# Optimization experiments

Measured on AMD Instinct MI355X. Metric: run time of the kernel, lower is better.

## Reference

```python
import jax, jax.numpy as jnp
import numpy as np
import math

B, S, D, O_DIM = 8, 2048, 1024, 1024

def setup_inputs() -> dict:
    key = jax.random.key(0)
    ks = jax.random.split(key, 4)
    scale = 1.0 / math.sqrt(D)
    return {
        "x": jax.random.normal(ks[0], (B, S, D), dtype=jnp.float32),
        "Wq": jax.random.normal(ks[1], (D, O_DIM), dtype=jnp.float32) * scale,
        "bq": jnp.zeros((O_DIM,), dtype=jnp.float32),
        "Wk": jax.random.normal(ks[2], (D, O_DIM), dtype=jnp.float32) * scale,
        "bk": jnp.zeros((O_DIM,), dtype=jnp.float32),
        "Wv": jax.random.normal(ks[3], (D, O_DIM), dtype=jnp.float32) * scale,
        "bv": jnp.zeros((O_DIM,), dtype=jnp.float32),
    }

def reference(x, Wq, bq, Wk, bk, Wv, bv):
    o_dim = Wq.shape[1]
    q = x @ Wq + bq  # [B,S,O]
    k = x @ Wk + bk
    v = x @ Wv + bv
    scores = jnp.einsum('bid,bjd->bij', q, k) / jnp.sqrt(jnp.float32(o_dim))
    n = scores.shape[1]
    # causal additive mask: upper triangle (j > i) gets -1e20 added
    causal = jnp.tril(jnp.ones((n, n), dtype=scores.dtype))
    scores = scores + (1.0 - causal) * (-1e20)
    probs = jax.nn.softmax(scores, axis=-1)
    return jnp.einsum('bij,bjd->bid', probs, v)
```

## Files before the change

### kernel.cpp

```cpp
#include <hip/hip_runtime.h>

#define BM 128
#define BN 128
#define BK 32

typedef unsigned short u16;
typedef unsigned int u32;
typedef __attribute__((ext_vector_type(8))) short short8;
typedef __attribute__((ext_vector_type(4))) float floatx4;

__device__ __forceinline__ u16 f2bf(float f) {
  u32 u = __float_as_uint(f);
  return (u16)((u + 0x7FFFu + ((u >> 16) & 1u)) >> 16);
}

__device__ __forceinline__ float bf2f(u16 b) {
  return __uint_as_float(((u32)b) << 16);
}

__device__ __forceinline__ void gload16(const void* g, void* l) {
  __builtin_amdgcn_global_load_lds((const __attribute__((address_space(1))) void*)g,
                                   (__attribute__((address_space(3))) void*)l, 16, 0, 0);
}

template<int BIAS_MODE, int SWZ>
__global__ __launch_bounds__(512, 2)
void gemm256(const u16* __restrict__ A, int lda,
             const u16* __restrict__ B, int ldb,
             u16* __restrict__ C, int ldc,
             const float* __restrict__ bias, int K)
{
  int bx = blockIdx.x, by = blockIdx.y;
  if (SWZ == 1) {
    const int c = gridDim.x >> 3;
    bx = (bx & 7) * c + (bx >> 3);
  } else if (SWZ == 2) {
    const u32 gx = gridDim.x;
    const u32 flat = (u32)by * gx + (u32)bx;
    const u32 j = flat & 7u, w = flat >> 3;
    const u32 rpx = gridDim.y >> 3;
    by = (int)(j * rpx + w / gx);
    bx = (int)(w % gx);
  }
  const int rb = by * 256, cb = bx * 256;

  __shared__ __align__(16) char lds[131072];

  const int t = threadIdx.x;
  const int lane = t & 63, wid = t >> 6;
  const int wr = wid >> 2, wc = wid & 3;

  floatx4 acc[8][4];
#pragma unroll
  for (int i = 0; i < 8; ++i)
#pragma unroll
    for (int j = 0; j < 4; ++j) acc[i][j] = (floatx4)(0.0f);

  const int sr = t >> 2;
  const int sl = (t & 3) ^ ((sr >> 1) & 3);
  const u16* Ag0 = A + (long)(rb + sr) * lda + sl * 8;
  const u16* Ag1 = A + (long)(rb + sr + 128) * lda + sl * 8;
  const u16* Bg0 = B + (long)(cb + sr) * ldb + sl * 8;
  const u16* Bg1 = B + (long)(cb + sr + 128) * ldb + sl * 8;

#define STAGE_A(T) { const long ko_ = (long)(T) * 32;                          \
    char* d_ = lds + (((T) & 3) << 15) + (wid << 10);                          \
    gload16(Ag0 + ko_, d_); gload16(Ag1 + ko_, d_ + 8192); }
#define STAGE_B(T) { const long ko_ = (long)(T) * 32;                          \
    char* d_ = lds + (((T) & 3) << 15) + 16384 + (wid << 10);                  \
    gload16(Bg0 + ko_, d_); gload16(Bg1 + ko_, d_ + 8192); }

  const int g = lane >> 4;
  int aoff[8], boff[4];
  const int arow = wr * 128 + (lane & 15);
  const int brow = wc * 64 + (lane & 15);
#pragma unroll
  for (int i = 0; i < 8; ++i) {
    const int ra = arow + i * 16;
    aoff[i] = ra * 64 + ((g ^ ((ra >> 1) & 3)) * 16);
  }
#pragma unroll
  for (int j = 0; j < 4; ++j) {
    const int rbq = brow + j * 16;
    boff[j] = rbq * 64 + ((g ^ ((rbq >> 1) & 3)) * 16);
  }

  const int NT = K / 32;

  STAGE_A(0); STAGE_B(0);
  STAGE_A(1); STAGE_B(1);
  STAGE_A(2); STAGE_B(2);
  asm volatile("s_waitcnt vmcnt(8)" ::: "memory");
  __builtin_amdgcn_s_barrier();
  asm volatile("" ::: "memory");

  for (int T = 0; T < NT; ++T) {
    const char* bufA = lds + ((T & 3) << 15);
    const char* bufB = bufA + 16384;

    if (T + 3 < NT) STAGE_A(T + 3);
    short8 a0[4], bfr[4];
#pragma unroll
    for (int i = 0; i < 4; ++i) a0[i] = *(const short8*)(bufA + aoff[i]);
#pragma unroll
    for (int j = 0; j < 4; ++j) bfr[j] = *(const short8*)(bufB + boff[j]);
    __builtin_amdgcn_s_setprio(1);
#pragma unroll
    for (int mi = 0; mi < 4; ++mi)
#pragma unroll
      for (int nj = 0; nj < 4; ++nj)
        acc[mi][nj] = __builtin_amdgcn_mfma_f32_16x16x32_bf16(a0[mi], bfr[nj], acc[mi][nj], 0, 0, 0);
    __builtin_amdgcn_s_setprio(0);

    if (T + 3 < NT) STAGE_B(T + 3);
    short8 a1[4];
#pragma unroll
    for (int i = 0; i < 4; ++i) a1[i] = *(const short8*)(bufA + aoff[4 + i]);
    __builtin_amdgcn_s_setprio(1);
#pragma unroll
    for (int mi = 0; mi < 4; ++mi)
#pragma unroll
      for (int nj = 0; nj < 4; ++nj)
        acc[4 + mi][nj] = __builtin_amdgcn_mfma_f32_16x16x32_bf16(a1[mi], bfr[nj], acc[4 + mi][nj], 0, 0, 0);
    __builtin_amdgcn_s_setprio(0);

    asm volatile("" ::: "memory");
    if (T < NT - 3) {
      asm volatile("s_waitcnt vmcnt(8)" ::: "memory");
      __builtin_amdgcn_s_barrier();
    } else if (T == NT - 3) {
      asm volatile("s_waitcnt vmcnt(4)" ::: "memory");
      __builtin_amdgcn_s_barrier();
    } else if (T == NT - 2) {
      asm volatile("s_waitcnt vmcnt(0)" ::: "memory");
      __builtin_amdgcn_s_barrier();
    }
    asm volatile("" ::: "memory");
  }
#undef STAGE_A
#undef STAGE_B

#pragma unroll
  for (int mi = 0; mi < 8; ++mi) {
    const int r0 = rb + wr * 128 + mi * 16 + (lane >> 4) * 4;
#pragma unroll
    for (int nj = 0; nj < 4; ++nj) {
      const int c = cb + wc * 64 + nj * 16 + (lane & 15);
      float bc = 0.0f;
      if (BIAS_MODE == 1) bc = bias[c];
#pragma unroll
      for (int e = 0; e < 4; ++e) {
        const int r = r0 + e;
        float val = acc[mi][nj][e] + bc;
        if (BIAS_MODE == 2) val += bias[r];
        C[(long)r * ldc + c] = f2bf(val);
      }
    }
  }
}

template<int BIAS_MODE, bool OUT_BF16, bool CAUSAL, bool KLIMIT, int SWZ>
__global__ __launch_bounds__(256)
void gemm_nt(const u16* __restrict__ A, int lda, long strideA,
             const u16* __restrict__ B, int ldb, long strideB,
             void* __restrict__ Cv, int ldc, long strideC,
             const float* __restrict__ bias, float scale,
             int M, int N, int K)
{
  int bx = blockIdx.x;
  int by = blockIdx.y;
  if (SWZ == 1) {
    const int c = gridDim.x >> 3;
    bx = (bx & 7) * c + (bx >> 3);
  } else if (SWZ == 2) {
    const u32 gx = gridDim.x;
    const u32 flat = (u32)by * gx + (u32)bx;
    const u32 j = flat & 7u;
    const u32 w = flat >> 3;
    const u32 rpx = gridDim.y >> 3;
    by = (int)(j * rpx + w / gx);
    bx = (int)(w % gx);
  } else if (SWZ == 3) {
    by = gridDim.y - 1 - by;
  }
  const int rb = by * BM;
  const int cb = bx * BN;
  if (CAUSAL && cb > rb + (BM - 1)) return;

  A += (long)blockIdx.z * strideA;
  B += (long)blockIdx.z * strideB;
  const long coff = (long)blockIdx.z * strideC;

  __shared__ u16 As[BM * BK];
  __shared__ u16 Bs[BN * BK];

  const int t = threadIdx.x;
  const int lane = t & 63;
  const int wid = t >> 6;
  const int wr = wid >> 1, wc = wid & 1;

  floatx4 acc[4][4];
#pragma unroll
  for (int i = 0; i < 4; ++i)
#pragma unroll
    for (int j = 0; j < 4; ++j) acc[i][j] = (floatx4)(0.0f);

  const int srow = t >> 2;
  const int schunk = (t & 3) ^ ((srow >> 1) & 3);
  const u16* Ag0 = A + (long)(rb + srow) * lda + schunk * 8;
  const u16* Ag1 = A + (long)(rb + srow + 64) * lda + schunk * 8;
  const u16* Bg0 = B + (long)(cb + srow) * ldb + schunk * 8;
  const u16* Bg1 = B + (long)(cb + srow + 64) * ldb + schunk * 8;
  char* AsW = (char*)As + wid * 1024;
  char* BsW = (char*)Bs + wid * 1024;

  const int arow = wr * 64 + (lane & 15);
  const int brow = wc * 64 + (lane & 15);
  const int rchunk = lane >> 4;
  int aoff[4], boff[4];
#pragma unroll
  for (int i = 0; i < 4; ++i) {
    const int ra = arow + i * 16;
    aoff[i] = ra * 64 + ((rchunk ^ ((ra >> 1) & 3)) * 16);
    const int rbq = brow + i * 16;
    boff[i] = rbq * 64 + ((rchunk ^ ((rbq >> 1) & 3)) * 16);
  }

  int kend = K;
  if (KLIMIT) kend = (rb + BM < K) ? (rb + BM) : K;
  const int ktiles = kend / BK;

  for (int kt = 0; kt < ktiles; ++kt) {
    const long ko = (long)kt * BK;
    gload16(Ag0 + ko, AsW);
    gload16(Ag1 + ko, AsW + 4096);
    gload16(Bg0 + ko, BsW);
    gload16(Bg1 + ko, BsW + 4096);
    __syncthreads();
    short8 af[4], bfr[4];
#pragma unroll
    for (int i = 0; i < 4; ++i) {
      af[i]  = *(const short8*)((const char*)As + aoff[i]);
      bfr[i] = *(const short8*)((const char*)Bs + boff[i]);
    }
#pragma unroll
    for (int mi = 0; mi < 4; ++mi)
#pragma unroll
      for (int nj = 0; nj < 4; ++nj)
        acc[mi][nj] = __builtin_amdgcn_mfma_f32_16x16x32_bf16(af[mi], bfr[nj], acc[mi][nj], 0, 0, 0);
    __syncthreads();
  }

#pragma unroll
  for (int mi = 0; mi < 4; ++mi) {
    const int r0 = rb + wr * 64 + mi * 16 + (lane >> 4) * 4;
#pragma unroll
    for (int nj = 0; nj < 4; ++nj) {
      const int c = cb + wc * 64 + nj * 16 + (lane & 15);
      float bc = 0.0f;
      if (BIAS_MODE == 1) bc = bias[c];
#pragma unroll
      for (int e = 0; e < 4; ++e) {
        const int r = r0 + e;
        float val = acc[mi][nj][e] * scale + bc;
        if (BIAS_MODE == 2) val += bias[r];
        const long idx = coff + (long)r * ldc + c;
        if (OUT_BF16) ((u16*)Cv)[idx] = f2bf(val);
        else          ((float*)Cv)[idx] = val;
      }
    }
  }
}

__global__ __launch_bounds__(256)
void softmax_causal_bf16(u16* __restrict__ Pp, int n, long stride)
{
  const int i = blockIdx.x;
  u16* row = Pp + (long)blockIdx.y * stride + (long)i * n;
  const int t = threadIdx.x;
  const int lane = t & 63, wid = t >> 6;
  const int jb = t * 8;

  float v[8];
  const bool any = (jb <= i);
  if (any) {
    short8 sv = *(const short8*)(row + jb);
#pragma unroll
    for (int e = 0; e < 8; ++e) v[e] = bf2f((u16)sv[e]);
  } else {
#pragma unroll
    for (int e = 0; e < 8; ++e) v[e] = 0.0f;
  }

  float mx = -3.0e38f;
#pragma unroll
  for (int e = 0; e < 8; ++e) if (any && jb + e <= i) mx = fmaxf(mx, v[e]);
#pragma unroll
  for (int off = 32; off > 0; off >>= 1) mx = fmaxf(mx, __shfl_xor(mx, off));
  __shared__ float red[8];
  if (lane == 0) red[wid] = mx;
  __syncthreads();
  mx = fmaxf(fmaxf(red[0], red[1]), fmaxf(red[2], red[3]));

  float s = 0.0f;
#pragma unroll
  for (int e = 0; e < 8; ++e) {
    float p = (any && jb + e <= i) ? __expf(v[e] - mx) : 0.0f;
    v[e] = p; s += p;
  }
#pragma unroll
  for (int off = 32; off > 0; off >>= 1) s += __shfl_xor(s, off);
  if (lane == 0) red[4 + wid] = s;
  __syncthreads();
  s = red[4] + red[5] + red[6] + red[7];
  const float inv = 1.0f / s;

  short8 o;
#pragma unroll
  for (int e = 0; e < 8; ++e) o[e] = (short)f2bf(v[e] * inv);
  *(short8*)(row + jb) = o;
}

__global__ __launch_bounds__(256)
void transpose_conv(const float* __restrict__ W, u16* __restrict__ WT, int dim)
{
  __shared__ float tile[32][33];
  const int tx = threadIdx.x & 31;
  const int ty = threadIdx.x >> 5;
  const int c0 = blockIdx.x * 32;
  const int r0 = blockIdx.y * 32;
#pragma unroll
  for (int i = 0; i < 4; ++i)
    tile[ty + 8 * i][tx] = W[(long)(r0 + ty + 8 * i) * dim + c0 + tx];
  __syncthreads();
#pragma unroll
  for (int i = 0; i < 4; ++i)
    WT[(long)(c0 + ty + 8 * i) * dim + r0 + tx] = f2bf(tile[tx][ty + 8 * i]);
}

__global__ __launch_bounds__(256)
void conv_bf16(const float* __restrict__ X, u16* __restrict__ Xb, long n8)
{
  const long i = (long)blockIdx.x * 256 + threadIdx.x;
  if (i >= n8) return;
  const float4* s = (const float4*)X + i * 2;
  float4 a = s[0], b = s[1];
  short8 o;
  o[0] = (short)f2bf(a.x); o[1] = (short)f2bf(a.y);
  o[2] = (short)f2bf(a.z); o[3] = (short)f2bf(a.w);
  o[4] = (short)f2bf(b.x); o[5] = (short)f2bf(b.y);
  o[6] = (short)f2bf(b.z); o[7] = (short)f2bf(b.w);
  ((short8*)Xb)[i] = o;
}

__global__ __launch_bounds__(256)
void pack_bias2(const float* __restrict__ b0, const float* __restrict__ b1,
                float* __restrict__ dst, int n)
{
  const int i = blockIdx.x * 256 + threadIdx.x;
  if (i < n) dst[i] = b0[i];
  else if (i < 2 * n) dst[i] = b1[i - n];
}

extern "C" void kernel_launch(void* const* d_in, const int* in_sizes, int n_in,
                              void* d_out, int out_size, void* d_ws, size_t ws_size,
                              hipStream_t stream)
{
  const int Bb = 8, S = 2048, Dd = 1024, Od = 1024;
  const int M = Bb * S;

  const float* x  = (const float*)d_in[0];
  const float* Wq = (const float*)d_in[1];
  const float* bq = (const float*)d_in[2];
  const float* Wk = (const float*)d_in[3];
  const float* bk = (const float*)d_in[4];
  const float* Wv = (const float*)d_in[5];
  const float* bv = (const float*)d_in[6];
  float* out = (float*)d_out;

  char* ws = (char*)d_ws;
  u16* xb   = (u16*)(ws);
  u16* qk   = (u16*)(ws + 33554432L);
  u16* vT   = (u16*)(ws + 100663296L);
  u16* WqkT = (u16*)(ws + 134217728L);
  u16* WvT  = (u16*)(ws + 138412032L);
  float* bqk = (float*)(ws + 140509184L);
  const size_t attn_base = 140517376UL;

  conv_bf16<<<dim3(8192), dim3(256), 0, stream>>>(x, xb, (long)M * Dd / 8);
  transpose_conv<<<dim3(32, 32), dim3(256), 0, stream>>>(Wq, WqkT, Dd);
  transpose_conv<<<dim3(32, 32), dim3(256), 0, stream>>>(Wk, WqkT + (long)Od * Dd, Dd);
  transpose_conv<<<dim3(32, 32), dim3(256), 0, stream>>>(Wv, WvT, Dd);
  pack_bias2<<<dim3(8), dim3(256), 0, stream>>>(bq, bk, bqk, Od);

  gemm256<1, 2><<<dim3(2 * Od / 256, M / 256), dim3(512), 0, stream>>>(
      xb, Dd, WqkT, Dd, qk, 2 * Od, bqk, Dd);
  gemm256<2, 1><<<dim3(M / 256, Od / 256), dim3(512), 0, stream>>>(
      WvT, Dd, xb, Dd, vT, M, bv, Dd);

  const u16* qb = qk;
  const u16* kb = qk + Od;
  const int ldqk = 2 * Od;
  const long strideQK = (long)S * ldqk;
  const long sS = (long)S * S;

  u16* scores;
  int g;
  if (ws_size >= attn_base + 8UL * (size_t)sS * sizeof(u16)) {
    scores = (u16*)(ws + attn_base);
    g = 8;
  } else {
    scores = xb;
    g = 4;
  }

  dim3 blk(256);
  const float sc = 0.03125f;
  for (int b0 = 0; b0 < Bb; b0 += g) {
    const int gz = (b0 + g <= Bb) ? g : (Bb - b0);
    gemm_nt<0, true, true, false, 0><<<dim3(S / BN, S / BM, gz), blk, 0, stream>>>(
        qb + (long)b0 * strideQK, ldqk, strideQK,
        kb + (long)b0 * strideQK, ldqk, strideQK,
        scores, S, sS, nullptr, sc, S, S, Od);
    softmax_causal_bf16<<<dim3(S, gz), blk, 0, stream>>>(scores, S, sS);
    gemm_nt<0, false, false, true, 3><<<dim3(Od / BN, S / BM, gz), blk, 0, stream>>>(
        scores, S, sS, vT + (long)b0 * S, M, (long)S,
        out + (long)b0 * S * Od, Od, (long)S * Od, nullptr, 1.0f, S, Od, S);
  }
}
```

Baseline: 439.4 us.

## Use 256-tile GEMM for causal scores and split-K atomics for PV

New measurement: 473.7 us. 7.8% more time.

```diff
diff --git a/kernel.cpp b/kernel.cpp
--- a/kernel.cpp
+++ b/kernel.cpp
@@ -23,12 +23,12 @@
                                    (__attribute__((address_space(3))) void*)l, 16, 0, 0);
 }
 
-template<int BIAS_MODE, int SWZ>
+template<int BIAS_MODE, bool CAUSAL, int SWZ>
 __global__ __launch_bounds__(512, 2)
-void gemm256(const u16* __restrict__ A, int lda,
-             const u16* __restrict__ B, int ldb,
-             u16* __restrict__ C, int ldc,
-             const float* __restrict__ bias, int K)
+void gemm256(const u16* __restrict__ A, int lda, long strideA,
+             const u16* __restrict__ B, int ldb, long strideB,
+             u16* __restrict__ C, int ldc, long strideC,
+             const float* __restrict__ bias, float scale, int K)
 {
   int bx = blockIdx.x, by = blockIdx.y;
   if (SWZ == 1) {
@@ -43,6 +43,11 @@
     bx = (int)(w % gx);
   }
   const int rb = by * 256, cb = bx * 256;
+  if (CAUSAL && cb > rb + 255) return;
+
+  A += (long)blockIdx.z * strideA;
+  B += (long)blockIdx.z * strideB;
+  const long coff = (long)blockIdx.z * strideC;
 
   __shared__ __align__(16) char lds[131072];
 
@@ -151,15 +156,15 @@
 #pragma unroll
       for (int e = 0; e < 4; ++e) {
         const int r = r0 + e;
-        float val = acc[mi][nj][e] + bc;
+        float val = acc[mi][nj][e] * scale + bc;
         if (BIAS_MODE == 2) val += bias[r];
-        C[(long)r * ldc + c] = f2bf(val);
+        C[coff + (long)r * ldc + c] = f2bf(val);
       }
     }
   }
 }
 
-template<int BIAS_MODE, bool OUT_BF16, bool CAUSAL, bool KLIMIT, int SWZ>
+template<int BIAS_MODE, bool OUT_BF16, bool CAUSAL, bool KLIMIT, int SWZ, int SPLITK>
 __global__ __launch_bounds__(256)
 void gemm_nt(const u16* __restrict__ A, int lda, long strideA,
              const u16* __restrict__ B, int ldb, long strideB,
@@ -169,6 +174,8 @@
 {
   int bx = blockIdx.x;
   int by = blockIdx.y;
+  int ks = 0;
+  if (SPLITK > 1) { ks = by % SPLITK; by /= SPLITK; }
   if (SWZ == 1) {
     const int c = gridDim.x >> 3;
     bx = (bx & 7) * c + (bx >> 3);
@@ -181,11 +188,20 @@
     by = (int)(j * rpx + w / gx);
     bx = (int)(w % gx);
   } else if (SWZ == 3) {
-    by = gridDim.y - 1 - by;
+    by = (gridDim.y / SPLITK) - 1 - by;
   }
   const int rb = by * BM;
   const int cb = bx * BN;
   if (CAUSAL && cb > rb + (BM - 1)) return;
+
+  int kend = K;
+  if (KLIMIT) kend = (rb + BM < K) ? (rb + BM) : K;
+  int klo = 0, khi = kend;
+  if (SPLITK > 1) {
+    klo = ks * 1024;
+    khi = (kend < klo + 1024) ? kend : (klo + 1024);
+    if (klo >= khi) return;
+  }
 
   A += (long)blockIdx.z * strideA;
   B += (long)blockIdx.z * strideB;
@@ -226,11 +242,7 @@
     boff[i] = rbq * 64 + ((rchunk ^ ((rbq >> 1) & 3)) * 16);
   }
 
-  int kend = K;
-  if (KLIMIT) kend = (rb + BM < K) ? (rb + BM) : K;
-  const int ktiles = kend / BK;
-
-  for (int kt = 0; kt < ktiles; ++kt) {
+  for (int kt = klo / BK; kt < khi / BK; ++kt) {
     const long ko = (long)kt * BK;
     gload16(Ag0 + ko, AsW);
     gload16(Ag1 + ko, AsW + 4096);
@@ -265,8 +277,9 @@
         float val = acc[mi][nj][e] * scale + bc;
         if (BIAS_MODE == 2) val += bias[r];
         const long idx = coff + (long)r * ldc + c;
-        if (OUT_BF16) ((u16*)Cv)[idx] = f2bf(val);
-        else          ((float*)Cv)[idx] = val;
+        if (SPLITK > 1)      atomicAdd((float*)Cv + idx, val);
+        else if (OUT_BF16)   ((u16*)Cv)[idx] = f2bf(val);
+        else                 ((float*)Cv)[idx] = val;
       }
     }
   }
@@ -362,6 +375,14 @@
   else if (i < 2 * n) dst[i] = b1[i - n];
 }
 
+__global__ __launch_bounds__(256)
+void zero_f4(float4* __restrict__ p, long n4)
+{
+  const long stride = (long)gridDim.x * 256;
+  for (long i = (long)blockIdx.x * 256 + threadIdx.x; i < n4; i += stride)
+    p[i] = make_float4(0.f, 0.f, 0.f, 0.f);
+}
+
 extern "C" void kernel_launch(void* const* d_in, const int* in_sizes, int n_in,
                               void* d_out, int out_size, void* d_ws, size_t ws_size,
                               hipStream_t stream)
@@ -387,16 +408,17 @@
   float* bqk = (float*)(ws + 140509184L);
   const size_t attn_base = 140517376UL;
 
+  zero_f4<<<dim3(2048), dim3(256), 0, stream>>>((float4*)out, (long)out_size / 4);
   conv_bf16<<<dim3(8192), dim3(256), 0, stream>>>(x, xb, (long)M * Dd / 8);
   transpose_conv<<<dim3(32, 32), dim3(256), 0, stream>>>(Wq, WqkT, Dd);
   transpose_conv<<<dim3(32, 32), dim3(256), 0, stream>>>(Wk, WqkT + (long)Od * Dd, Dd);
   transpose_conv<<<dim3(32, 32), dim3(256), 0, stream>>>(Wv, WvT, Dd);
   pack_bias2<<<dim3(8), dim3(256), 0, stream>>>(bq, bk, bqk, Od);
 
-  gemm256<1, 2><<<dim3(2 * Od / 256, M / 256), dim3(512), 0, stream>>>(
-      xb, Dd, WqkT, Dd, qk, 2 * Od, bqk, Dd);
-  gemm256<2, 1><<<dim3(M / 256, Od / 256), dim3(512), 0, stream>>>(
-      WvT, Dd, xb, Dd, vT, M, bv, Dd);
+  gemm256<1, false, 2><<<dim3(2 * Od / 256, M / 256), dim3(512), 0, stream>>>(
+      xb, Dd, 0L, WqkT, Dd, 0L, qk, 2 * Od, 0L, bqk, 1.0f, Dd);
+  gemm256<2, false, 1><<<dim3(M / 256, Od / 256), dim3(512), 0, stream>>>(
+      WvT, Dd, 0L, xb, Dd, 0L, vT, M, 0L, bv, 1.0f, Dd);
 
   const u16* qb = qk;
   const u16* kb = qk + Od;
@@ -418,12 +440,12 @@
   const float sc = 0.03125f;
   for (int b0 = 0; b0 < Bb; b0 += g) {
     const int gz = (b0 + g <= Bb) ? g : (Bb - b0);
-    gemm_nt<0, true, true, false, 0><<<dim3(S / BN, S / BM, gz), blk, 0, stream>>>(
+    gemm256<0, true, 0><<<dim3(S / 256, S / 256, gz), dim3(512), 0, stream>>>(
         qb + (long)b0 * strideQK, ldqk, strideQK,
         kb + (long)b0 * strideQK, ldqk, strideQK,
-        scores, S, sS, nullptr, sc, S, S, Od);
+        scores, S, sS, nullptr, sc, Od);
     softmax_causal_bf16<<<dim3(S, gz), blk, 0, stream>>>(scores, S, sS);
-    gemm_nt<0, false, false, true, 3><<<dim3(Od / BN, S / BM, gz), blk, 0, stream>>>(
+    gemm_nt<0, false, false, true, 3, 2><<<dim3(Od / BN, (S / BM) * 2, gz), blk, 0, stream>>>(
         scores, S, sS, vT + (long)b0 * S, M, (long)S,
         out + (long)b0 * S * Od, Od, (long)S * Od, nullptr, 1.0f, S, Od, S);
   }
```

## Use pipelined 256x256 gemm kernel for attention GEMMs and fuse weight transposes

Applied to the files above, without the earlier changes.

Result: faster. 407.2 us (-7.3%).

```diff
diff --git a/kernel.cpp b/kernel.cpp
--- a/kernel.cpp
+++ b/kernel.cpp
@@ -1,8 +1,4 @@
 #include <hip/hip_runtime.h>
-
-#define BM 128
-#define BN 128
-#define BK 32
 
 typedef unsigned short u16;
 typedef unsigned int u32;
@@ -23,12 +19,12 @@
                                    (__attribute__((address_space(3))) void*)l, 16, 0, 0);
 }
 
-template<int BIAS_MODE, int SWZ>
+template<int BIAS_MODE, bool OUT_BF16, bool CAUSAL, bool KLIMIT, int SWZ>
 __global__ __launch_bounds__(512, 2)
-void gemm256(const u16* __restrict__ A, int lda,
-             const u16* __restrict__ B, int ldb,
-             u16* __restrict__ C, int ldc,
-             const float* __restrict__ bias, int K)
+void gemm256(const u16* __restrict__ A, int lda, long strideA,
+             const u16* __restrict__ B, int ldb, long strideB,
+             void* __restrict__ Cv, int ldc, long strideC,
+             const float* __restrict__ bias, float scale, int K)
 {
   int bx = blockIdx.x, by = blockIdx.y;
   if (SWZ == 1) {
@@ -43,6 +39,11 @@
     bx = (int)(w % gx);
   }
   const int rb = by * 256, cb = bx * 256;
+  if (CAUSAL && cb > rb + 255) return;
+
+  A += (long)blockIdx.z * strideA;
+  B += (long)blockIdx.z * strideB;
+  const long coff = (long)blockIdx.z * strideC;
 
   __shared__ __align__(16) char lds[131072];
 
@@ -85,7 +86,9 @@
     boff[j] = rbq * 64 + ((g ^ ((rbq >> 1) & 3)) * 16);
   }
 
-  const int NT = K / 32;
+  int kend = K;
+  if (KLIMIT) kend = (rb + 256 < K) ? (rb + 256) : K;
+  const int NT = kend / 32;
 
   STAGE_A(0); STAGE_B(0);
   STAGE_A(1); STAGE_B(1);
@@ -151,117 +154,6 @@
 #pragma unroll
       for (int e = 0; e < 4; ++e) {
         const int r = r0 + e;
-        float val = acc[mi][nj][e] + bc;
-        if (BIAS_MODE == 2) val += bias[r];
-        C[(long)r * ldc + c] = f2bf(val);
-      }
-    }
-  }
-}
-
-template<int BIAS_MODE, bool OUT_BF16, bool CAUSAL, bool KLIMIT, int SWZ>
-__global__ __launch_bounds__(256)
-void gemm_nt(const u16* __restrict__ A, int lda, long strideA,
-             const u16* __restrict__ B, int ldb, long strideB,
-             void* __restrict__ Cv, int ldc, long strideC,
-             const float* __restrict__ bias, float scale,
-             int M, int N, int K)
-{
-  int bx = blockIdx.x;
-  int by = blockIdx.y;
-  if (SWZ == 1) {
-    const int c = gridDim.x >> 3;
-    bx = (bx & 7) * c + (bx >> 3);
-  } else if (SWZ == 2) {
-    const u32 gx = gridDim.x;
-    const u32 flat = (u32)by * gx + (u32)bx;
-    const u32 j = flat & 7u;
-    const u32 w = flat >> 3;
-    const u32 rpx = gridDim.y >> 3;
-    by = (int)(j * rpx + w / gx);
-    bx = (int)(w % gx);
-  } else if (SWZ == 3) {
-    by = gridDim.y - 1 - by;
-  }
-  const int rb = by * BM;
-  const int cb = bx * BN;
-  if (CAUSAL && cb > rb + (BM - 1)) return;
-
-  A += (long)blockIdx.z * strideA;
-  B += (long)blockIdx.z * strideB;
-  const long coff = (long)blockIdx.z * strideC;
-
-  __shared__ u16 As[BM * BK];
-  __shared__ u16 Bs[BN * BK];
-
-  const int t = threadIdx.x;
-  const int lane = t & 63;
-  const int wid = t >> 6;
-  const int wr = wid >> 1, wc = wid & 1;
-
-  floatx4 acc[4][4];
-#pragma unroll
-  for (int i = 0; i < 4; ++i)
-#pragma unroll
-    for (int j = 0; j < 4; ++j) acc[i][j] = (floatx4)(0.0f);
-
-  const int srow = t >> 2;
-  const int schunk = (t & 3) ^ ((srow >> 1) & 3);
-  const u16* Ag0 = A + (long)(rb + srow) * lda + schunk * 8;
-  const u16* Ag1 = A + (long)(rb + srow + 64) * lda + schunk * 8;
-  const u16* Bg0 = B + (long)(cb + srow) * ldb + schunk * 8;
-  const u16* Bg1 = B + (long)(cb + srow + 64) * ldb + schunk * 8;
-  char* AsW = (char*)As + wid * 1024;
-  char* BsW = (char*)Bs + wid * 1024;
-
-  const int arow = wr * 64 + (lane & 15);
-  const int brow = wc * 64 + (lane & 15);
-  const int rchunk = lane >> 4;
-  int aoff[4], boff[4];
-#pragma unroll
-  for (int i = 0; i < 4; ++i) {
-    const int ra = arow + i * 16;
-    aoff[i] = ra * 64 + ((rchunk ^ ((ra >> 1) & 3)) * 16);
-    const int rbq = brow + i * 16;
-    boff[i] = rbq * 64 + ((rchunk ^ ((rbq >> 1) & 3)) * 16);
-  }
-
-  int kend = K;
-  if (KLIMIT) kend = (rb + BM < K) ? (rb + BM) : K;
-  const int ktiles = kend / BK;
-
-  for (int kt = 0; kt < ktiles; ++kt) {
-    const long ko = (long)kt * BK;
-    gload16(Ag0 + ko, AsW);
-    gload16(Ag1 + ko, AsW + 4096);
-    gload16(Bg0 + ko, BsW);
-    gload16(Bg1 + ko, BsW + 4096);
-    __syncthreads();
-    short8 af[4], bfr[4];
-#pragma unroll
-    for (int i = 0; i < 4; ++i) {
-      af[i]  = *(const short8*)((const char*)As + aoff[i]);
-      bfr[i] = *(const short8*)((const char*)Bs + boff[i]);
-    }
-#pragma unroll
-    for (int mi = 0; mi < 4; ++mi)
-#pragma unroll
-      for (int nj = 0; nj < 4; ++nj)
-        acc[mi][nj] = __builtin_amdgcn_mfma_f32_16x16x32_bf16(af[mi], bfr[nj], acc[mi][nj], 0, 0, 0);
-    __syncthreads();
-  }
-
-#pragma unroll
-  for (int mi = 0; mi < 4; ++mi) {
-    const int r0 = rb + wr * 64 + mi * 16 + (lane >> 4) * 4;
-#pragma unroll
-    for (int nj = 0; nj < 4; ++nj) {
-      const int c = cb + wc * 64 + nj * 16 + (lane & 15);
-      float bc = 0.0f;
-      if (BIAS_MODE == 1) bc = bias[c];
-#pragma unroll
-      for (int e = 0; e < 4; ++e) {
-        const int r = r0 + e;
         float val = acc[mi][nj][e] * scale + bc;
         if (BIAS_MODE == 2) val += bias[r];
         const long idx = coff + (long)r * ldc + c;
@@ -322,8 +214,16 @@
 }
 
 __global__ __launch_bounds__(256)
-void transpose_conv(const float* __restrict__ W, u16* __restrict__ WT, int dim)
-{
+void transpose_conv3(const float* __restrict__ Wq, const float* __restrict__ Wk,
+                     const float* __restrict__ Wv, u16* __restrict__ WqkT,
+                     u16* __restrict__ WvT, int dim)
+{
+  const float* W;
+  u16* WT;
+  if (blockIdx.z == 0)      { W = Wq; WT = WqkT; }
+  else if (blockIdx.z == 1) { W = Wk; WT = WqkT + (long)dim * dim; }
+  else                      { W = Wv; WT = WvT; }
+
   __shared__ float tile[32][33];
   const int tx = threadIdx.x & 31;
   const int ty = threadIdx.x >> 5;
@@ -388,15 +288,13 @@
   const size_t attn_base = 140517376UL;
 
   conv_bf16<<<dim3(8192), dim3(256), 0, stream>>>(x, xb, (long)M * Dd / 8);
-  transpose_conv<<<dim3(32, 32), dim3(256), 0, stream>>>(Wq, WqkT, Dd);
-  transpose_conv<<<dim3(32, 32), dim3(256), 0, stream>>>(Wk, WqkT + (long)Od * Dd, Dd);
-  transpose_conv<<<dim3(32, 32), dim3(256), 0, stream>>>(Wv, WvT, Dd);
+  transpose_conv3<<<dim3(32, 32, 3), dim3(256), 0, stream>>>(Wq, Wk, Wv, WqkT, WvT, Dd);
   pack_bias2<<<dim3(8), dim3(256), 0, stream>>>(bq, bk, bqk, Od);
 
-  gemm256<1, 2><<<dim3(2 * Od / 256, M / 256), dim3(512), 0, stream>>>(
-      xb, Dd, WqkT, Dd, qk, 2 * Od, bqk, Dd);
-  gemm256<2, 1><<<dim3(M / 256, Od / 256), dim3(512), 0, stream>>>(
-      WvT, Dd, xb, Dd, vT, M, bv, Dd);
+  gemm256<1, true, false, false, 2><<<dim3(2 * Od / 256, M / 256), dim3(512), 0, stream>>>(
+      xb, Dd, 0L, WqkT, Dd, 0L, qk, 2 * Od, 0L, bqk, 1.0f, Dd);
+  gemm256<2, true, false, false, 1><<<dim3(M / 256, Od / 256), dim3(512), 0, stream>>>(
+      WvT, Dd, 0L, xb, Dd, 0L, vT, M, 0L, bv, 1.0f, Dd);
 
   const u16* qb = qk;
   const u16* kb = qk + Od;
@@ -414,17 +312,16 @@
     g = 4;
   }
 
-  dim3 blk(256);
   const float sc = 0.03125f;
   for (int b0 = 0; b0 < Bb; b0 += g) {
     const int gz = (b0 + g <= Bb) ? g : (Bb - b0);
-    gemm_nt<0, true, true, false, 0><<<dim3(S / BN, S / BM, gz), blk, 0, stream>>>(
+    gemm256<0, true, true, false, 0><<<dim3(S / 256, S / 256, gz), dim3(512), 0, stream>>>(
         qb + (long)b0 * strideQK, ldqk, strideQK,
         kb + (long)b0 * strideQK, ldqk, strideQK,
-        scores, S, sS, nullptr, sc, S, S, Od);
-    softmax_causal_bf16<<<dim3(S, gz), blk, 0, stream>>>(scores, S, sS);
-    gemm_nt<0, false, false, true, 3><<<dim3(Od / BN, S / BM, gz), blk, 0, stream>>>(
+        scores, S, sS, nullptr, sc, Od);
+    softmax_causal_bf16<<<dim3(S, gz), dim3(256), 0, stream>>>(scores, S, sS);
+    gemm256<0, false, false, true, 0><<<dim3(Od / 256, S / 256, gz), dim3(512), 0, stream>>>(
         scores, S, sS, vT + (long)b0 * S, M, (long)S,
-        out + (long)b0 * S * Od, Od, (long)S * Od, nullptr, 1.0f, S, Od, S);
-  }
-}
+        out + (long)b0 * S * Od, Od, (long)S * Od, nullptr, 1.0f, S);
+  }
+}
```
